# Optimization experiments

Hardware: AMD Instinct MI355X
Metric: run time of the kernel (lower is better)

The kernel has to match this reference:

```python
import jax, jax.numpy as jnp
import numpy as np

B, L, E, H, K = 256, 500, 300, 10, 5  # batch, doc_len, word_embedding, h1, num_aspects


def setup_inputs() -> dict:
    key = jax.random.key(0)
    k1, k2, k3 = jax.random.split(key, 3)
    review = jax.random.normal(k1, (B, L, E), dtype=jnp.float32)
    # params initialized uniform(-0.01, 0.01) as in the torch module
    aspProj = jax.random.uniform(k2, (K, E, H), dtype=jnp.float32, minval=-0.01, maxval=0.01)
    aspEmbed = jax.random.uniform(k3, (K, 3 * H), dtype=jnp.float32, minval=-0.01, maxval=0.01)
    return {"review": review, "aspProj": aspProj, "aspEmbed": aspEmbed}


def reference(review, aspProj, aspEmbed):
    # project review into each aspect subspace: (K, B, L, H)
    proj = jnp.einsum('ble,keh->kblh', review, aspProj)
    # pad seq dim by 1 on each side, build window-3 unfold.
    # torch unfold(1,3,1) yields (B, L, H, 3) then reshape to (B, L, 3*H),
    # i.e. feature layout is (h_index, window_offset) -- match by stacking
    # window offsets on the LAST axis before the reshape.
    padded = jnp.pad(proj, ((0, 0), (0, 0), (1, 1), (0, 0)))
    windows = jnp.stack([padded[:, :, i:i + L, :] for i in range(3)], axis=-1)  # (K,B,L,H,3)
    windows = windows.reshape(K, windows.shape[1], L, 3 * H)  # (K,B,L,3H)
    # attention logits per position, softmax over the WHOLE sequence dim
    scores = jnp.einsum('kblf,kf->kbl', windows, aspEmbed)
    attn = jax.nn.softmax(scores, axis=-1)  # (K,B,L)
    # attention-weighted sum over sequence -> aspect representation
    rep = jnp.einsum('kblh,kbl->kbh', proj, attn)  # (K,B,H)
    batch_aspAttn = jnp.transpose(attn, (1, 0, 2))  # (B,K,L)
    batch_aspRep = jnp.transpose(rep, (1, 0, 2))    # (B,K,H)
    return (batch_aspAttn, batch_aspRep)
```

## Files before the change

kernel.cpp:

```cpp
#include <hip/hip_runtime.h>

#define BB 256
#define LL 500
#define EE 300
#define HH 10
#define KK 5
#define NF 50
#define NT 512
#define NWAVE 8

#define MP 512
#define CK 32
#define NCH 10
#define AP 40
#define BP 328
#define PP 53
#define NR4 75
#define NA4 3750

#define B_OFF    (2 * MP * AP * 2)
#define B_BYTES  (64 * BP * 2)
#define SD_OFF   (MP * PP * 4)
#define RED_OFF  (SD_OFF + 3 * KK * MP * 4)
#define REP_OFF  (RED_OFF + KK * NWAVE * 4)
#define EMB_OFF  (REP_OFF + NWAVE * NF * 4)
#define SMEM_BYTES (EMB_OFF + KK * 3 * HH * 4)

typedef __attribute__((ext_vector_type(8))) short short8;
typedef __attribute__((ext_vector_type(4))) float f32x4;

__device__ __forceinline__ unsigned int f2bf(float x) {
    unsigned int u = __float_as_uint(x);
    return (u + 0x7FFFu + ((u >> 16) & 1u)) >> 16;
}

__global__ __launch_bounds__(NT, 2) void anr_mfma3(
    const float* __restrict__ review,
    const float* __restrict__ aspProj,
    const float* __restrict__ aspEmbed,
    float* __restrict__ out)
{
    __shared__ __align__(16) char smem[SMEM_BYTES];
    short* B16   = (short*)(smem + B_OFF);
    float* proj  = (float*)smem;
    float* s_d   = (float*)(smem + SD_OFF);
    float* s_red = (float*)(smem + RED_OFF);
    float* s_rep = (float*)(smem + REP_OFF);
    float* s_emb = (float*)(smem + EMB_OFF);

    const int tid  = threadIdx.x;
    const int b    = blockIdx.x;
    const int lane = tid & 63;
    const int w    = tid >> 6;
    const int quad = lane >> 4;
    const int m16  = lane & 15;
    const int q    = tid & 7;
    const int r0   = tid >> 3;

    for (int j = tid; j < B_BYTES / 4; j += NT)
        ((int*)(smem + B_OFF))[j] = 0;
    __syncthreads();

    const float4* rev4 = (const float4*)review + (size_t)b * LL * NR4;
    const float4* rp[8];
#pragma unroll
    for (int i = 0; i < 8; ++i) {
        int r = r0 + 64 * i;
        rp[i] = rev4 + (size_t)((r < LL) ? r : (LL - 1)) * NR4;
    }

    const float4* ap4 = (const float4*)aspProj;
    float4 bt[8];
#pragma unroll
    for (int i = 0; i < 8; ++i) {
        int idx = tid + NT * i;
        bt[i] = ap4[(idx < NA4) ? idx : (NA4 - 1)];
    }
    float embv = aspEmbed[(tid < KK * 3 * HH) ? tid : 0];
    float4 ld[8];
#pragma unroll
    for (int i = 0; i < 8; ++i) ld[i] = rp[i][q];

#pragma unroll
    for (int i = 0; i < 8; ++i) {
        int idx = tid + NT * i;
        if (idx < NA4) {
            float vv[4] = {bt[i].x, bt[i].y, bt[i].z, bt[i].w};
#pragma unroll
            for (int cm = 0; cm < 4; ++cm) {
                int jj   = 4 * idx + cm;
                int kasp = jj / (EE * HH);
                int rr   = jj - kasp * (EE * HH);
                int e    = rr / HH;
                int h    = rr - e * HH;
                B16[(kasp * HH + h) * BP + e] = (short)f2bf(vv[cm]);
            }
        }
    }
    if (tid < KK * 3 * HH) s_emb[tid] = embv;

    {
        short* An = (short*)smem;
#pragma unroll
        for (int i = 0; i < 8; ++i) {
            int r = r0 + 64 * i;
            uint2 pk;
            pk.x = f2bf(ld[i].x) | (f2bf(ld[i].y) << 16);
            pk.y = f2bf(ld[i].z) | (f2bf(ld[i].w) << 16);
            *(uint2*)&An[r * AP + q * 4] = pk;
        }
    }
    __syncthreads();

    f32x4 acc[4][4];
#pragma unroll
    for (int mi = 0; mi < 4; ++mi)
#pragma unroll
        for (int ni = 0; ni < 4; ++ni)
            acc[mi][ni] = (f32x4){0.f, 0.f, 0.f, 0.f};

#pragma unroll
    for (int c = 0; c < NCH; ++c) {
        if (c + 1 < NCH) {
            int fq = 8 * (c + 1) + q;
            if (fq > NR4 - 1) fq = NR4 - 1;
#pragma unroll
            for (int i = 0; i < 8; ++i) ld[i] = rp[i][fq];
        }
        const short* Ac = (const short*)smem + (c & 1) * (MP * AP);
        short8 af[4], bf[4];
#pragma unroll
        for (int mi = 0; mi < 4; ++mi)
            af[mi] = *(const short8*)&Ac[(w * 64 + mi * 16 + m16) * AP + quad * 8];
#pragma unroll
        for (int ni = 0; ni < 4; ++ni)
            bf[ni] = *(const short8*)&B16[(ni * 16 + m16) * BP + c * CK + quad * 8];
#pragma unroll
        for (int mi = 0; mi < 4; ++mi)
#pragma unroll
            for (int ni = 0; ni < 4; ++ni)
                acc[mi][ni] = __builtin_amdgcn_mfma_f32_16x16x32_bf16(
                    af[mi], bf[ni], acc[mi][ni], 0, 0, 0);
        if (c + 1 < NCH) {
            short* An = (short*)smem + ((c + 1) & 1) * (MP * AP);
#pragma unroll
            for (int i = 0; i < 8; ++i) {
                int r = r0 + 64 * i;
                uint2 pk;
                pk.x = f2bf(ld[i].x) | (f2bf(ld[i].y) << 16);
                pk.y = f2bf(ld[i].z) | (f2bf(ld[i].w) << 16);
                *(uint2*)&An[r * AP + q * 4] = pk;
            }
            __syncthreads();
        }
    }

    __syncthreads();
#pragma unroll
    for (int mi = 0; mi < 4; ++mi) {
#pragma unroll
        for (int ni = 0; ni < 4; ++ni) {
            int col = ni * 16 + m16;
            if (col < NF) {
                int row = w * 64 + mi * 16 + quad * 4;
#pragma unroll
                for (int r = 0; r < 4; ++r)
                    proj[(row + r) * PP + col] = acc[mi][ni][r];
            }
        }
    }
    __syncthreads();

    const int l  = tid;
    const bool vl = (l < LL);

    float pr[NF];
#pragma unroll
    for (int f = 0; f < NF; ++f) pr[f] = proj[l * PP + f];

    float d0[KK], d1[KK], d2[KK];
#pragma unroll
    for (int k = 0; k < KK; ++k) {
        float a0 = 0.f, a1 = 0.f, a2 = 0.f;
#pragma unroll
        for (int h = 0; h < HH; ++h) {
            float x = pr[k * HH + h];
            a0 = fmaf(x, s_emb[k * 3 * HH + 3 * h + 0], a0);
            a1 = fmaf(x, s_emb[k * 3 * HH + 3 * h + 1], a1);
            a2 = fmaf(x, s_emb[k * 3 * HH + 3 * h + 2], a2);
        }
        d0[k] = vl ? a0 : 0.f;
        d1[k] = vl ? a1 : 0.f;
        d2[k] = vl ? a2 : 0.f;
    }
#pragma unroll
    for (int k = 0; k < KK; ++k) {
        s_d[(0 * KK + k) * MP + l] = d0[k];
        s_d[(1 * KK + k) * MP + l] = d1[k];
        s_d[(2 * KK + k) * MP + l] = d2[k];
    }
    __syncthreads();

    const int lp1 = (l + 1 < MP) ? l + 1 : MP - 1;
    float sc[KK];
#pragma unroll
    for (int k = 0; k < KK; ++k) {
        float t0 = (l >= 1) ? s_d[(0 * KK + k) * MP + l - 1] : 0.f;
        float t1 = s_d[(1 * KK + k) * MP + l];
        float t2 = s_d[(2 * KK + k) * MP + lp1];
        sc[k] = vl ? (t0 + t1 + t2) : -1e30f;
    }

    float mx[KK];
#pragma unroll
    for (int k = 0; k < KK; ++k) {
        float m = sc[k];
        for (int s = 32; s > 0; s >>= 1) m = fmaxf(m, __shfl_xor(m, s, 64));
        if (lane == 0) s_red[k * NWAVE + w] = m;
    }
    __syncthreads();
#pragma unroll
    for (int k = 0; k < KK; ++k) {
        float m = s_red[k * NWAVE + 0];
#pragma unroll
        for (int ww = 1; ww < NWAVE; ++ww) m = fmaxf(m, s_red[k * NWAVE + ww]);
        mx[k] = m;
    }
    __syncthreads();
    float ex[KK], sm[KK];
#pragma unroll
    for (int k = 0; k < KK; ++k) {
        ex[k] = __expf(sc[k] - mx[k]);
        float s = ex[k];
        for (int sh = 32; sh > 0; sh >>= 1) s += __shfl_xor(s, sh, 64);
        if (lane == 0) s_red[k * NWAVE + w] = s;
    }
    __syncthreads();
#pragma unroll
    for (int k = 0; k < KK; ++k) {
        float s = 0.f;
#pragma unroll
        for (int ww = 0; ww < NWAVE; ++ww) s += s_red[k * NWAVE + ww];
        sm[k] = s;
    }

#pragma unroll
    for (int k = 0; k < KK; ++k) {
        float wk = ex[k] / sm[k];
        if (vl) out[((size_t)b * KK + k) * LL + l] = wk;
#pragma unroll
        for (int h = 0; h < HH; ++h) {
            float v = pr[k * HH + h] * wk;
            for (int sh = 32; sh > 0; sh >>= 1) v += __shfl_xor(v, sh, 64);
            if (lane == 0) s_rep[w * NF + k * HH + h] = v;
        }
    }
    __syncthreads();
    if (tid < NF) {
        float s = 0.f;
#pragma unroll
        for (int ww = 0; ww < NWAVE; ++ww) s += s_rep[ww * NF + tid];
        out[(size_t)BB * KK * LL + (size_t)b * NF + tid] = s;
    }
}

extern "C" void kernel_launch(void* const* d_in, const int* in_sizes, int n_in,
                              void* d_out, int out_size, void* d_ws, size_t ws_size,
                              hipStream_t stream) {
    const float* review   = (const float*)d_in[0];
    const float* aspProj  = (const float*)d_in[1];
    const float* aspEmbed = (const float*)d_in[2];
    float* out = (float*)d_out;

    anr_mfma3<<<dim3(BB), dim3(NT), 0, stream>>>(review, aspProj, aspEmbed, out);
}
```

Measured before the change: 238.8 us.

## Split fused kernel into weight-prep, row-split GEMM, and attention kernels

Splits the single per-batch kernel into three launches: a tiny kernel that converts aspProj to transposed bf16 in workspace, a GEMM kernel that gives each batch four blocks of 128 rows with 64-wide K chunks, and an attention/softmax kernel that reads the projection back from global workspace. The aim is more blocks and higher occupancy for the memory-bound projection phase, since the old design ran only 256 large blocks on a GPU with many CUs. In exchange it adds two extra launches and a global round-trip for the 50-wide projection per row.

Result: slower. 252.2 us (+5.6%).

```diff
diff --git a/kernel.cpp b/kernel.cpp
--- a/kernel.cpp
+++ b/kernel.cpp
@@ -6,25 +6,16 @@
 #define HH 10
 #define KK 5
 #define NF 50
-#define NT 512
 #define NWAVE 8
 
-#define MP 512
-#define CK 32
-#define NCH 10
-#define AP 40
 #define BP 328
-#define PP 53
+#define AP 72
+#define PW 52
+#define MPB 512
 #define NR4 75
-#define NA4 3750
-
-#define B_OFF    (2 * MP * AP * 2)
-#define B_BYTES  (64 * BP * 2)
-#define SD_OFF   (MP * PP * 4)
-#define RED_OFF  (SD_OFF + 3 * KK * MP * 4)
-#define REP_OFF  (RED_OFF + KK * NWAVE * 4)
-#define EMB_OFF  (REP_OFF + NWAVE * NF * 4)
-#define SMEM_BYTES (EMB_OFF + KK * 3 * HH * 4)
+
+#define WS_BT_BYTES  (64 * BP * 2)
+#define WS_PROJ_OFF  65536
 
 typedef __attribute__((ext_vector_type(8))) short short8;
 typedef __attribute__((ext_vector_type(4))) float f32x4;
@@ -34,118 +25,90 @@
     return (u + 0x7FFFu + ((u >> 16) & 1u)) >> 16;
 }
 
-__global__ __launch_bounds__(NT, 2) void anr_mfma3(
+__global__ void k0_bt(const float* __restrict__ aspProj, short* __restrict__ btw) {
+    int j = blockIdx.x * 512 + threadIdx.x;
+    if (j >= 64 * BP) return;
+    int n = j / BP, e = j - n * BP;
+    float v = 0.f;
+    if (n < NF && e < EE) v = aspProj[(n / HH) * (EE * HH) + e * HH + (n - (n / HH) * HH)];
+    btw[j] = (short)f2bf(v);
+}
+
+__global__ __launch_bounds__(512, 4) void k1_gemm(
     const float* __restrict__ review,
-    const float* __restrict__ aspProj,
-    const float* __restrict__ aspEmbed,
-    float* __restrict__ out)
+    const short* __restrict__ btw,
+    float* __restrict__ projw)
 {
-    __shared__ __align__(16) char smem[SMEM_BYTES];
-    short* B16   = (short*)(smem + B_OFF);
-    float* proj  = (float*)smem;
-    float* s_d   = (float*)(smem + SD_OFF);
-    float* s_red = (float*)(smem + RED_OFF);
-    float* s_rep = (float*)(smem + REP_OFF);
-    float* s_emb = (float*)(smem + EMB_OFF);
+    __shared__ short sB[64 * BP];
+    __shared__ short sA[2][128 * AP];
 
     const int tid  = threadIdx.x;
-    const int b    = blockIdx.x;
+    const int b    = blockIdx.x >> 2;
+    const int rq   = blockIdx.x & 3;
     const int lane = tid & 63;
     const int w    = tid >> 6;
     const int quad = lane >> 4;
     const int m16  = lane & 15;
-    const int q    = tid & 7;
-    const int r0   = tid >> 3;
-
-    for (int j = tid; j < B_BYTES / 4; j += NT)
-        ((int*)(smem + B_OFF))[j] = 0;
-    __syncthreads();
+    const int q    = tid & 15;
+    const int r0   = tid >> 4;
+
+    {
+        const int4* src = (const int4*)btw;
+        int4* dst = (int4*)sB;
+        for (int j = tid; j < WS_BT_BYTES / 16; j += 512) dst[j] = src[j];
+    }
 
     const float4* rev4 = (const float4*)review + (size_t)b * LL * NR4;
-    const float4* rp[8];
-#pragma unroll
-    for (int i = 0; i < 8; ++i) {
-        int r = r0 + 64 * i;
+    const float4* rp[4];
+#pragma unroll
+    for (int i = 0; i < 4; ++i) {
+        int r = rq * 128 + r0 + 32 * i;
         rp[i] = rev4 + (size_t)((r < LL) ? r : (LL - 1)) * NR4;
     }
 
-    const float4* ap4 = (const float4*)aspProj;
-    float4 bt[8];
-#pragma unroll
-    for (int i = 0; i < 8; ++i) {
-        int idx = tid + NT * i;
-        bt[i] = ap4[(idx < NA4) ? idx : (NA4 - 1)];
-    }
-    float embv = aspEmbed[(tid < KK * 3 * HH) ? tid : 0];
-    float4 ld[8];
-#pragma unroll
-    for (int i = 0; i < 8; ++i) ld[i] = rp[i][q];
-
-#pragma unroll
-    for (int i = 0; i < 8; ++i) {
-        int idx = tid + NT * i;
-        if (idx < NA4) {
-            float vv[4] = {bt[i].x, bt[i].y, bt[i].z, bt[i].w};
-#pragma unroll
-            for (int cm = 0; cm < 4; ++cm) {
-                int jj   = 4 * idx + cm;
-                int kasp = jj / (EE * HH);
-                int rr   = jj - kasp * (EE * HH);
-                int e    = rr / HH;
-                int h    = rr - e * HH;
-                B16[(kasp * HH + h) * BP + e] = (short)f2bf(vv[cm]);
-            }
-        }
-    }
-    if (tid < KK * 3 * HH) s_emb[tid] = embv;
-
-    {
-        short* An = (short*)smem;
-#pragma unroll
-        for (int i = 0; i < 8; ++i) {
-            int r = r0 + 64 * i;
-            uint2 pk;
-            pk.x = f2bf(ld[i].x) | (f2bf(ld[i].y) << 16);
-            pk.y = f2bf(ld[i].z) | (f2bf(ld[i].w) << 16);
-            *(uint2*)&An[r * AP + q * 4] = pk;
-        }
-    }
-    __syncthreads();
-
-    f32x4 acc[4][4];
-#pragma unroll
-    for (int mi = 0; mi < 4; ++mi)
-#pragma unroll
-        for (int ni = 0; ni < 4; ++ni)
-            acc[mi][ni] = (f32x4){0.f, 0.f, 0.f, 0.f};
-
-#pragma unroll
-    for (int c = 0; c < NCH; ++c) {
-        if (c + 1 < NCH) {
-            int fq = 8 * (c + 1) + q;
+    float4 ld[4];
+#pragma unroll
+    for (int i = 0; i < 4; ++i) ld[i] = rp[i][q];
+
+#pragma unroll
+    for (int i = 0; i < 4; ++i) {
+        int r = r0 + 32 * i;
+        uint2 pk;
+        pk.x = f2bf(ld[i].x) | (f2bf(ld[i].y) << 16);
+        pk.y = f2bf(ld[i].z) | (f2bf(ld[i].w) << 16);
+        *(uint2*)&sA[0][r * AP + q * 4] = pk;
+    }
+    __syncthreads();
+
+    f32x4 acc[4];
+#pragma unroll
+    for (int ni = 0; ni < 4; ++ni) acc[ni] = (f32x4){0.f, 0.f, 0.f, 0.f};
+
+#pragma unroll
+    for (int c = 0; c < 5; ++c) {
+        if (c + 1 < 5) {
+            int fq = (c + 1) * 16 + q;
             if (fq > NR4 - 1) fq = NR4 - 1;
 #pragma unroll
-            for (int i = 0; i < 8; ++i) ld[i] = rp[i][fq];
-        }
-        const short* Ac = (const short*)smem + (c & 1) * (MP * AP);
-        short8 af[4], bf[4];
-#pragma unroll
-        for (int mi = 0; mi < 4; ++mi)
-            af[mi] = *(const short8*)&Ac[(w * 64 + mi * 16 + m16) * AP + quad * 8];
-#pragma unroll
-        for (int ni = 0; ni < 4; ++ni)
-            bf[ni] = *(const short8*)&B16[(ni * 16 + m16) * BP + c * CK + quad * 8];
-#pragma unroll
-        for (int mi = 0; mi < 4; ++mi)
+            for (int i = 0; i < 4; ++i) ld[i] = rp[i][fq];
+        }
+        const short* Ac = sA[c & 1];
+#pragma unroll
+        for (int s = 0; s < 2; ++s) {
+            short8 af = *(const short8*)&Ac[(w * 16 + m16) * AP + s * 32 + quad * 8];
+            short8 bf[4];
 #pragma unroll
             for (int ni = 0; ni < 4; ++ni)
-                acc[mi][ni] = __builtin_amdgcn_mfma_f32_16x16x32_bf16(
-                    af[mi], bf[ni], acc[mi][ni], 0, 0, 0);
-        if (c + 1 < NCH) {
-            short* An = (short*)smem + ((c + 1) & 1) * (MP * AP);
-#pragma unroll
-            for (int i = 0; i < 8; ++i) {
-                int r = r0 + 64 * i;
+                bf[ni] = *(const short8*)&sB[(ni * 16 + m16) * BP + c * 64 + s * 32 + quad * 8];
+#pragma unroll
+            for (int ni = 0; ni < 4; ++ni)
+                acc[ni] = __builtin_amdgcn_mfma_f32_16x16x32_bf16(af, bf[ni], acc[ni], 0, 0, 0);
+        }
+        if (c + 1 < 5) {
+            short* An = sA[(c + 1) & 1];
+#pragma unroll
+            for (int i = 0; i < 4; ++i) {
+                int r = r0 + 32 * i;
                 uint2 pk;
                 pk.x = f2bf(ld[i].x) | (f2bf(ld[i].y) << 16);
                 pk.y = f2bf(ld[i].z) | (f2bf(ld[i].w) << 16);
@@ -155,28 +118,49 @@
         }
     }
 
-    __syncthreads();
-#pragma unroll
-    for (int mi = 0; mi < 4; ++mi) {
-#pragma unroll
-        for (int ni = 0; ni < 4; ++ni) {
-            int col = ni * 16 + m16;
-            if (col < NF) {
-                int row = w * 64 + mi * 16 + quad * 4;
-#pragma unroll
-                for (int r = 0; r < 4; ++r)
-                    proj[(row + r) * PP + col] = acc[mi][ni][r];
-            }
-        }
-    }
-    __syncthreads();
-
-    const int l  = tid;
-    const bool vl = (l < LL);
-
-    float pr[NF];
-#pragma unroll
-    for (int f = 0; f < NF; ++f) pr[f] = proj[l * PP + f];
+    float* pw = projw + (size_t)b * MPB * PW;
+    const int rowbase = rq * 128 + w * 16 + quad * 4;
+#pragma unroll
+    for (int ni = 0; ni < 4; ++ni) {
+        int col = ni * 16 + m16;
+        if (col < NF) {
+#pragma unroll
+            for (int r = 0; r < 4; ++r)
+                pw[(size_t)(rowbase + r) * PW + col] = acc[ni][r];
+        }
+    }
+}
+
+__global__ __launch_bounds__(512, 2) void k2_attn(
+    const float* __restrict__ projw,
+    const float* __restrict__ aspEmbed,
+    float* __restrict__ out)
+{
+    __shared__ float s_d[3 * KK * MPB];
+    __shared__ float s_red[KK * NWAVE];
+    __shared__ float s_rep[NWAVE * NF];
+    __shared__ float s_emb[KK * 3 * HH];
+
+    const int tid  = threadIdx.x;
+    const int b    = blockIdx.x;
+    const int lane = tid & 63;
+    const int w    = tid >> 6;
+    const int l    = tid;
+    const bool vl  = (l < LL);
+
+    if (tid < KK * 3 * HH) s_emb[tid] = aspEmbed[tid];
+
+    float4 prv[13];
+    const float4* pr4 = (const float4*)(projw + (size_t)b * MPB * PW + (size_t)l * PW);
+#pragma unroll
+    for (int i = 0; i < 13; ++i) prv[i] = pr4[i];
+    float pr[52];
+#pragma unroll
+    for (int i = 0; i < 13; ++i) {
+        pr[4 * i + 0] = prv[i].x; pr[4 * i + 1] = prv[i].y;
+        pr[4 * i + 2] = prv[i].z; pr[4 * i + 3] = prv[i].w;
+    }
+    __syncthreads();
 
     float d0[KK], d1[KK], d2[KK];
 #pragma unroll
@@ -195,19 +179,19 @@
     }
 #pragma unroll
     for (int k = 0; k < KK; ++k) {
-        s_d[(0 * KK + k) * MP + l] = d0[k];
-        s_d[(1 * KK + k) * MP + l] = d1[k];
-        s_d[(2 * KK + k) * MP + l] = d2[k];
-    }
-    __syncthreads();
-
-    const int lp1 = (l + 1 < MP) ? l + 1 : MP - 1;
+        s_d[(0 * KK + k) * MPB + l] = d0[k];
+        s_d[(1 * KK + k) * MPB + l] = d1[k];
+        s_d[(2 * KK + k) * MPB + l] = d2[k];
+    }
+    __syncthreads();
+
+    const int lp1 = (l + 1 < MPB) ? l + 1 : MPB - 1;
     float sc[KK];
 #pragma unroll
     for (int k = 0; k < KK; ++k) {
-        float t0 = (l >= 1) ? s_d[(0 * KK + k) * MP + l - 1] : 0.f;
-        float t1 = s_d[(1 * KK + k) * MP + l];
-        float t2 = s_d[(2 * KK + k) * MP + lp1];
+        float t0 = (l >= 1) ? s_d[(0 * KK + k) * MPB + l - 1] : 0.f;
+        float t1 = s_d[(1 * KK + k) * MPB + l];
+        float t2 = s_d[(2 * KK + k) * MPB + lp1];
         sc[k] = vl ? (t0 + t1 + t2) : -1e30f;
     }
 
@@ -270,7 +254,11 @@
     const float* review   = (const float*)d_in[0];
     const float* aspProj  = (const float*)d_in[1];
     const float* aspEmbed = (const float*)d_in[2];
-    float* out = (float*)d_out;
-
-    anr_mfma3<<<dim3(BB), dim3(NT), 0, stream>>>(review, aspProj, aspEmbed, out);
-}
+    float* out   = (float*)d_out;
+    short* btw   = (short*)d_ws;
+    float* projw = (float*)((char*)d_ws + WS_PROJ_OFF);
+
+    k0_bt  <<<dim3((64 * BP + 511) / 512), dim3(512), 0, stream>>>(aspProj, btw);
+    k1_gemm<<<dim3(BB * 4), dim3(512), 0, stream>>>(review, btw, projw);
+    k2_attn<<<dim3(BB), dim3(512), 0, stream>>>(projw, aspEmbed, out);
+}
```
